# Kernel tuning notes

Hardware: AMD Instinct MI355X
Metric: run time of the kernel (lower is better)

Reference implementation:

```python
import jax, jax.numpy as jnp
import numpy as np

POOL_SCALES = (1, 3, 6, 8)
CHANNELS = 256
BN_EPS = 1e-5


def _pool_matrix(in_size, out_size):
    # Row i averages input slots [floor(i*in/out), ceil((i+1)*in/out)) -- matches AdaptiveAvgPool2d.
    P = np.zeros((out_size, in_size), np.float32)
    for i in range(out_size):
        s = (i * in_size) // out_size
        e = -((-(i + 1) * in_size) // out_size)
        P[i, s:e] = 1.0 / (e - s)
    return jnp.asarray(P)


def _bn(x, g, b, m, v):
    # inference-mode BatchNorm2d on NCHW
    inv = g * jax.lax.rsqrt(v + BN_EPS)
    return x * inv[None, :, None, None] + (b - m * inv)[None, :, None, None]


def _conv1x1(x, w):
    # 1x1 conv == channel matmul: w [Cout, Cin], x [B, Cin, H, W]
    return jnp.einsum('oc,bchw->bohw', w, x)


def _ppm_concat(x):
    # x: [B, C, H, W] -> [B, C, sum(s*s)]
    B, C, H, W = x.shape
    outs = []
    for s in POOL_SCALES:
        Ph = _pool_matrix(H, s)
        Pw = _pool_matrix(W, s)
        pooled = jnp.einsum('ih,jw,bchw->bcij', Ph, Pw, x)
        outs.append(pooled.reshape(B, C, -1))
    return jnp.concatenate(outs, axis=2)


def setup_inputs() -> dict:
    key = jax.random.key(0)
    ks = jax.random.split(key, 24)
    B, Cl, Ch, Cmid, Cout, H, W = 8, 1024, 2048, 256, 2048, 64, 64
    return {
        'low_feats': jax.random.normal(ks[0], (B, Cl, H, W), jnp.float32),
        'high_feats': jax.random.normal(ks[1], (B, Ch, H, W), jnp.float32),
        'q_w': jax.random.normal(ks[2], (Cmid, Ch), jnp.float32) * 0.02,
        'q_g': jax.random.uniform(ks[3], (Cmid,), jnp.float32, 0.5, 1.5),
        'q_b': jax.random.normal(ks[4], (Cmid,), jnp.float32) * 0.1,
        'q_m': jax.random.normal(ks[5], (Cmid,), jnp.float32) * 0.1,
        'q_v': jax.random.uniform(ks[6], (Cmid,), jnp.float32, 0.5, 1.5),
        'k_w': jax.random.normal(ks[7], (Cmid, Cl), jnp.float32) * 0.02,
        'k_g': jax.random.uniform(ks[8], (Cmid,), jnp.float32, 0.5, 1.5),
        'k_b': jax.random.normal(ks[9], (Cmid,), jnp.float32) * 0.1,
        'k_m': jax.random.normal(ks[10], (Cmid,), jnp.float32) * 0.1,
        'k_v': jax.random.uniform(ks[11], (Cmid,), jnp.float32, 0.5, 1.5),
        'v_w': jax.random.normal(ks[12], (Cmid, Cl), jnp.float32) * 0.02,
        'v_b': jax.random.normal(ks[13], (Cmid,), jnp.float32) * 0.02,
        'o_w': jax.random.normal(ks[14], (Cout, Cmid), jnp.float32) * 0.02,
        'o_b': jax.random.normal(ks[15], (Cout,), jnp.float32) * 0.02,
        'bn_w': jax.random.normal(ks[16], (Cout, Cout + Ch), jnp.float32) * 0.02,
        'bn_g': jax.random.uniform(ks[17], (Cout,), jnp.float32, 0.5, 1.5),
        'bn_b': jax.random.normal(ks[18], (Cout,), jnp.float32) * 0.1,
        'bn_m': jax.random.normal(ks[19], (Cout,), jnp.float32) * 0.1,
        'bn_v': jax.random.uniform(ks[20], (Cout,), jnp.float32, 0.5, 1.5),
    }


def reference(low_feats, high_feats, q_w, q_g, q_b, q_m, q_v,
              k_w, k_g, k_b, k_m, k_v, v_w, v_b, o_w, o_b,
              bn_w, bn_g, bn_b, bn_m, bn_v):
    B, _, H, W = high_feats.shape
    # query: ConvModule (1x1 conv, BN, ReLU) on high-level feats; query_scale=1 -> no downsample
    q = jax.nn.relu(_bn(_conv1x1(high_feats, q_w), q_g, q_b, q_m, q_v))
    q = q.reshape(B, CHANNELS, H * W).transpose(0, 2, 1)  # [B, N, C]
    # key: ConvModule then pyramid-pooled; value: plain 1x1 conv then pyramid-pooled
    k = jax.nn.relu(_bn(_conv1x1(low_feats, k_w), k_g, k_b, k_m, k_v))
    k = _ppm_concat(k)  # [B, C, M]
    v = _conv1x1(low_feats, v_w) + v_b[None, :, None, None]
    v = _ppm_concat(v).transpose(0, 2, 1)  # [B, M, C]
    # matmul-normalized attention with pooled K/V (M = 110, tiny)
    sim = jnp.einsum('bnc,bcm->bnm', q, k) * (CHANNELS ** -0.5)
    sim = jax.nn.softmax(sim, axis=-1)
    ctx = jnp.einsum('bnm,bmc->bnc', sim, v)  # [B, N, C]
    ctx = ctx.transpose(0, 2, 1).reshape(B, CHANNELS, H, W)
    # out projection: plain 1x1 conv with bias
    ctx = _conv1x1(ctx, o_w) + o_b[None, :, None, None]  # [B, Cout, H, W]
    # single stage (query_scales=(1,)), stack+sum is identity
    # bottleneck: 1x1 conv (no bias) + BN, no activation
    fused = jnp.concatenate([ctx, high_feats], axis=1)
    out = _bn(_conv1x1(fused, bn_w), bn_g, bn_b, bn_m, bn_v)
    return out
```

## Files before the change

### kernel.cpp

```cpp
#include <hip/hip_runtime.h>
#include <hip/hip_bf16.h>

typedef unsigned int u32;
typedef unsigned short u16;
typedef short s16x8 __attribute__((ext_vector_type(8)));
typedef float f32x4 __attribute__((ext_vector_type(4)));
typedef u16 u16x4 __attribute__((ext_vector_type(4)));

__device__ __forceinline__ u16 f2b(float x) {
  u32 u = __float_as_uint(x);
  return (u16)((u + 0x7fffu + ((u >> 16) & 1u)) >> 16);
}
__device__ __forceinline__ float b2f(u16 x) { return __uint_as_float(((u32)x) << 16); }

__device__ __forceinline__ void gload16(const void* g, void* l) {
  __builtin_amdgcn_global_load_lds((const __attribute__((address_space(1))) u32*)g,
                                   (__attribute__((address_space(3))) u32*)l, 16, 0, 0);
}
__device__ __forceinline__ f32x4 mfma16(s16x8 a, s16x8 b, f32x4 c) {
  return __builtin_amdgcn_mfma_f32_16x16x32_bf16(a, b, c, 0, 0, 0);
}

template <int OUT_BF16>
__global__ __launch_bounds__(512, 2) void gemm256(
    const u16* __restrict__ A, long long sA, int lda,
    const u16* __restrict__ B1, long long sB1, int K1,
    const u16* __restrict__ B2, long long sB2, int K2,
    void* __restrict__ Cv, long long sC, int ldc,
    const float* __restrict__ bias, int bias_mode,
    int relu_limit, float alpha) {
  const int K = K1 + K2, nt = K >> 6;
  int tm, tn, b;
  {
    const int flat = blockIdx.x + gridDim.x * (blockIdx.y + gridDim.y * blockIdx.z);
    if (gridDim.z == 8) {
      const int slot = flat >> 3;
      b = flat & 7;
      tm = slot % gridDim.x;
      tn = slot / gridDim.x;
    } else { tm = blockIdx.x; tn = blockIdx.y; b = blockIdx.z; }
  }
  const u16* Ab = A + (size_t)b * sA + (size_t)tm * 256 * lda;
  const u16* B1b = B1 + (size_t)b * sB1 + (size_t)tn * 256 * K1;
  const u16* B2b = B2 ? (B2 + (size_t)b * sB2 + (size_t)tn * 256 * K2) : (const u16*)0;

  __shared__ __attribute__((aligned(128))) char lds[131072];

  const int tt = threadIdx.x, w = tt >> 6, l = tt & 63;
  const int wr = w >> 2, wc = w & 3;
  const int lr = l & 15, g16 = l >> 4;
  const int sxl = (lr & 7) << 4;

  auto stage_Aq = [&](int kt, int q) {
    const int bufB = (kt & 1) << 16;
    const int kk = kt << 6;
    const int lin = tt << 4;
    const int x = lin ^ (((lin >> 7) & 7) << 4);
    gload16(Ab + (size_t)((q << 6) + (x >> 7)) * lda + kk + ((x & 127) >> 1),
            lds + bufB + (q << 13) + (w << 10));
  };
  auto stage_Bh = [&](int kt, int h) {
    const int bufB = (kt & 1) << 16;
    const int kk = kt << 6;
    const u16* src; int ld, kcol;
    if (kk < K1) { src = B1b; ld = K1; kcol = kk; }
    else         { src = B2b; ld = K2; kcol = kk - K1; }
#pragma unroll
    for (int g = 0; g < 2; ++g) {
      const int lin = (g << 13) | (tt << 4);
      const int x = lin ^ (((lin >> 7) & 7) << 4);
      gload16(src + (size_t)((h << 7) + (x >> 7)) * ld + kcol + ((x & 127) >> 1),
              lds + bufB + 32768 + (h << 14) + (g << 13) + (w << 10));
    }
  };

  auto lda_frag = [&](const char* Al, int h, int kk, s16x8* af) {
#pragma unroll
    for (int i = 0; i < 4; ++i) {
      const int row = wr * 128 + (h * 4 + i) * 16 + lr;
      af[i] = *reinterpret_cast<const s16x8*>(
          Al + (row << 7) + (((kk << 6) | (g16 << 4)) ^ sxl));
    }
  };
  auto ldb_frag = [&](const char* Bl, int kk, s16x8* bf) {
#pragma unroll
    for (int n = 0; n < 4; ++n) {
      const int row = wc * 64 + n * 16 + lr;
      bf[n] = *reinterpret_cast<const s16x8*>(
          Bl + (row << 7) + (((kk << 6) | (g16 << 4)) ^ sxl));
    }
  };

  f32x4 acc[8][4] = {};

  auto mfma_q = [&](int h, const s16x8* af, const s16x8* bf) {
    __builtin_amdgcn_s_setprio(1);
#pragma unroll
    for (int i = 0; i < 4; ++i)
#pragma unroll
      for (int n = 0; n < 4; ++n)
        acc[h * 4 + i][n] = mfma16(af[i], bf[n], acc[h * 4 + i][n]);
    __builtin_amdgcn_s_setprio(0);
  };

  stage_Aq(0, 0); stage_Aq(0, 2); stage_Bh(0, 0); stage_Bh(0, 1);
  stage_Aq(0, 1); stage_Aq(0, 3);
  if (nt > 1) {
    stage_Aq(1, 0); stage_Aq(1, 2); stage_Bh(1, 0); stage_Bh(1, 1);
    asm volatile("s_waitcnt vmcnt(6)" ::: "memory");
  } else {
    asm volatile("s_waitcnt vmcnt(0)" ::: "memory");
  }
  __builtin_amdgcn_s_barrier();

  for (int t = 0; t < nt; ++t) {
    const char* Al = lds + ((t & 1) << 16);
    const char* Bl = Al + 32768;
    s16x8 bf0[4], bf1[4], af[4];

    lda_frag(Al, 0, 0, af);
    ldb_frag(Bl, 0, bf0);
    if (t + 1 < nt) { stage_Aq(t + 1, 1); stage_Aq(t + 1, 3); }
    __builtin_amdgcn_s_barrier();
    asm volatile("s_waitcnt lgkmcnt(0)" ::: "memory");
    mfma_q(0, af, bf0);
    __builtin_amdgcn_s_barrier();

    lda_frag(Al, 0, 1, af);
    ldb_frag(Bl, 1, bf1);
    __builtin_amdgcn_s_barrier();
    asm volatile("s_waitcnt lgkmcnt(0)" ::: "memory");
    mfma_q(0, af, bf1);
    __builtin_amdgcn_s_barrier();

    lda_frag(Al, 1, 0, af);
    if (t + 2 < nt) { stage_Aq(t + 2, 0); stage_Aq(t + 2, 2); stage_Bh(t + 2, 0); }
    __builtin_amdgcn_s_barrier();
    asm volatile("s_waitcnt lgkmcnt(0)" ::: "memory");
    mfma_q(1, af, bf0);
    __builtin_amdgcn_s_barrier();

    lda_frag(Al, 1, 1, af);
    if (t + 2 < nt) stage_Bh(t + 2, 1);
    __builtin_amdgcn_s_barrier();
    asm volatile("s_waitcnt lgkmcnt(0)" ::: "memory");
    mfma_q(1, af, bf1);
    if (t + 1 < nt) {
      if (t + 2 < nt) asm volatile("s_waitcnt vmcnt(6)" ::: "memory");
      else            asm volatile("s_waitcnt vmcnt(0)" ::: "memory");
    }
    __builtin_amdgcn_s_barrier();
  }

  const int li = g16 * 4;
#pragma unroll
  for (int m = 0; m < 8; ++m) {
    const int row = tm * 256 + wr * 128 + m * 16 + li;
#pragma unroll
    for (int j = 0; j < 4; ++j) {
      const int col = tn * 256 + wc * 64 + j * 16 + lr;
      const float bc = (bias_mode == 1) ? bias[col] : 0.f;
#pragma unroll
      for (int i = 0; i < 4; ++i) {
        float v = acc[m][j][i] * alpha;
        v += (bias_mode == 2) ? bias[row + i] : bc;
        if (col < relu_limit) v = fmaxf(v, 0.f);
        const size_t idx = (size_t)b * sC + (size_t)(row + i) * ldc + col;
        if (OUT_BF16) ((u16*)Cv)[idx] = f2b(v);
        else          ((float*)Cv)[idx] = v;
      }
    }
  }
}

template <int OUT_BF16>
__global__ __launch_bounds__(256) void gemm_bt(
    const u16* __restrict__ A, long long sA, int lda,
    const u16* __restrict__ B1, long long sB1, int K1,
    const u16* __restrict__ B2, long long sB2, int K2,
    void* __restrict__ Cv, long long sC, int ldc,
    const float* __restrict__ bias, int bias_mode,
    int relu_limit, float alpha) {
  const int K = K1 + K2;
  const int b = blockIdx.z;
  const int tm = blockIdx.x, tn = blockIdx.y;
  const u16* Ab = A + (size_t)b * sA;
  const u16* B1b = B1 + (size_t)b * sB1;
  const u16* B2b = B2 ? (B2 + (size_t)b * sB2) : (const u16*)0;

  __shared__ u16 As[128 * 32];
  __shared__ u16 Bs[128 * 32];

  const int t = threadIdx.x;
  const int w = t >> 6, l = t & 63;
  const int wr = w >> 1, wc = w & 1;
  const int srow = w * 16 + (l >> 2);
  const int scol = (l & 3) * 8;
  u16* AsW = As + w * 512;
  u16* BsW = Bs + w * 512;

  f32x4 acc[4][4] = {};
  const int lr = l & 15, lk = (l >> 4) * 8;

  for (int kk = 0; kk < K; kk += 32) {
    __syncthreads();
    {
      const u16* g0 = Ab + (size_t)(tm * 128 + srow) * lda + (kk + scol);
      gload16(g0, AsW);
      gload16(g0 + (size_t)64 * lda, AsW + 2048);
    }
    {
      const u16* bb; int ld, kloc;
      if (kk < K1) { bb = B1b; ld = K1; kloc = kk; }
      else         { bb = B2b; ld = K2; kloc = kk - K1; }
      const u16* g0 = bb + (size_t)(tn * 128 + srow) * ld + (kloc + scol);
      gload16(g0, BsW);
      gload16(g0 + (size_t)64 * ld, BsW + 2048);
    }
    __syncthreads();
    s16x8 af[4], bfr[4];
#pragma unroll
    for (int m = 0; m < 4; ++m)
      af[m] = *reinterpret_cast<const s16x8*>(&As[(wr * 64 + m * 16 + lr) * 32 + lk]);
#pragma unroll
    for (int j = 0; j < 4; ++j)
      bfr[j] = *reinterpret_cast<const s16x8*>(&Bs[(wc * 64 + j * 16 + lr) * 32 + lk]);
#pragma unroll
    for (int m = 0; m < 4; ++m)
#pragma unroll
      for (int j = 0; j < 4; ++j)
        acc[m][j] = mfma16(af[m], bfr[j], acc[m][j]);
  }

  const int li = (l >> 4) * 4;
#pragma unroll
  for (int m = 0; m < 4; ++m) {
    const int row = tm * 128 + wr * 64 + m * 16 + li;
#pragma unroll
    for (int j = 0; j < 4; ++j) {
      const int col = tn * 128 + wc * 64 + j * 16 + lr;
      const float bc = (bias_mode == 1) ? bias[col] : 0.f;
#pragma unroll
      for (int i = 0; i < 4; ++i) {
        float v = acc[m][j][i] * alpha;
        v += (bias_mode == 2) ? bias[row + i] : bc;
        if (col < relu_limit) v = fmaxf(v, 0.f);
        const size_t idx = (size_t)b * sC + (size_t)(row + i) * ldc + col;
        if (OUT_BF16) ((u16*)Cv)[idx] = f2b(v);
        else          ((float*)Cv)[idx] = v;
      }
    }
  }
}

__global__ __launch_bounds__(512) void attn_fused(
    const u16* __restrict__ qT,
    const u16* __restrict__ Kp,
    const u16* __restrict__ Vp,
    u16* __restrict__ ctxT) {
  const int qb = blockIdx.x, b = blockIdx.y;
  const int tt = threadIdx.x, w = tt >> 6, l = tt & 63;
  const int lr = l & 15, hi = l >> 4;
  __shared__ __attribute__((aligned(128))) char lds[131072];

  const char* KpG = (const char*)(Kp + (size_t)b * 32768);
  const char* VpG = (const char*)(Vp + (size_t)b * 32768);
#pragma unroll
  for (int g = 0; g < 8; ++g) {
    const int lin = (g * 512 + tt) << 4;
    gload16(KpG + (lin ^ (((lin >> 9) & 7) << 4)), lds + g * 8192 + w * 1024);
  }
#pragma unroll
  for (int g = 0; g < 8; ++g) {
    const int lin = (g * 512 + tt) << 4;
    gload16(VpG + (lin ^ (((lin >> 8) & 7) << 4)), lds + 65536 + g * 8192 + w * 1024);
  }

  const u16* qG = qT + ((size_t)b * 4096 + qb * 128 + w * 16 + lr) * 256 + hi * 8;
  s16x8 qf[8];
#pragma unroll
  for (int kk = 0; kk < 8; ++kk)
    qf[kk] = *reinterpret_cast<const s16x8*>(qG + kk * 32);

  asm volatile("s_waitcnt vmcnt(0)" ::: "memory");
  __syncthreads();

  f32x4 ps[8] = {};
  for (int kk = 0; kk < 8; ++kk) {
#pragma unroll
    for (int j = 0; j < 8; ++j) {
      const int y = (j * 16 + lr) * 512 + kk * 64 + hi * 16;
      const s16x8 kf = *reinterpret_cast<const s16x8*>(lds + (y ^ (((y >> 9) & 7) << 4)));
      ps[j] = mfma16(qf[kk], kf, ps[j]);
    }
  }
  __syncthreads();

#pragma unroll
  for (int i = 0; i < 4; ++i) {
    float m0 = -1e30f;
#pragma unroll
    for (int j = 0; j < 7; ++j) {
      float v = ps[j][i] * 0.0625f;
      if (j == 6 && lr >= 14) v = -1e30f;
      m0 = fmaxf(m0, v);
    }
#pragma unroll
    for (int off = 8; off; off >>= 1) m0 = fmaxf(m0, __shfl_xor(m0, off, 16));
    float s0 = 0.f;
#pragma unroll
    for (int j = 0; j < 7; ++j) {
      const float v = ps[j][i] * 0.0625f;
      const float ev = (j == 6 && lr >= 14) ? 0.f : __expf(v - m0);
      ps[j][i] = ev;
      s0 += ev;
    }
    ps[7][i] = 0.f;
#pragma unroll
    for (int off = 8; off; off >>= 1) s0 += __shfl_xor(s0, off, 16);
    const float inv = 1.f / s0;
#pragma unroll
    for (int j = 0; j < 8; ++j) ps[j][i] *= inv;
  }

  char* PL = lds + w * 4096;
#pragma unroll
  for (int j = 0; j < 8; ++j)
#pragma unroll
    for (int i = 0; i < 4; ++i) {
      const int n = hi * 4 + i, m = j * 16 + lr;
      const int y = n * 256 + m * 2;
      *reinterpret_cast<u16*>(PL + (y ^ ((n & 7) << 4))) = f2b(ps[j][i]);
    }
  __syncthreads();

  f32x4 pc[16] = {};
  const char* VL = lds + 65536;
#pragma unroll
  for (int kk = 0; kk < 4; ++kk) {
    const int ya = lr * 256 + kk * 64 + hi * 16;
    const s16x8 pa = *reinterpret_cast<const s16x8*>(PL + (ya ^ ((lr & 7) << 4)));
#pragma unroll
    for (int jc = 0; jc < 16; ++jc) {
      const int y = (jc * 16 + lr) * 256 + kk * 64 + hi * 16;
      const s16x8 vf = *reinterpret_cast<const s16x8*>(VL + (y ^ (((y >> 8) & 7) << 4)));
      pc[jc] = mfma16(pa, vf, pc[jc]);
    }
  }

  u16* outp = ctxT + ((size_t)b * 4096 + qb * 128 + w * 16) * 256;
#pragma unroll
  for (int jc = 0; jc < 16; ++jc)
#pragma unroll
    for (int i = 0; i < 4; ++i)
      outp[(size_t)(hi * 4 + i) * 256 + jc * 16 + lr] = f2b(pc[jc][i]);
}

__global__ __launch_bounds__(256) void transpose_cvt(
    const float* __restrict__ in, u16* __restrict__ out, int R, int C) {
  const int b = blockIdx.z;
  in += (size_t)b * R * C;
  out += (size_t)b * R * C;
  const int ct = blockIdx.x, rt = blockIdx.y;
  __shared__ float tile[64][65];
  const int t = threadIdx.x;
  {
    const int c4 = (t & 15) * 4, r0 = t >> 4;
    const float* src = in + (size_t)(rt * 64 + r0) * C + ct * 64 + c4;
#pragma unroll
    for (int i = 0; i < 4; ++i) {
      const float4 v = *reinterpret_cast<const float4*>(src + (size_t)(i * 16) * C);
      tile[r0 + i * 16][c4 + 0] = v.x; tile[r0 + i * 16][c4 + 1] = v.y;
      tile[r0 + i * 16][c4 + 2] = v.z; tile[r0 + i * 16][c4 + 3] = v.w;
    }
  }
  __syncthreads();
  {
    const int r4 = (t & 15) * 4, c0 = t >> 4;
    u16* dst = out + (size_t)(ct * 64 + c0) * R + rt * 64 + r4;
#pragma unroll
    for (int i = 0; i < 4; ++i) {
      u16x4 o;
      o.x = f2b(tile[r4 + 0][c0 + i * 16]);
      o.y = f2b(tile[r4 + 1][c0 + i * 16]);
      o.z = f2b(tile[r4 + 2][c0 + i * 16]);
      o.w = f2b(tile[r4 + 3][c0 + i * 16]);
      *reinterpret_cast<u16x4*>(dst + (size_t)(i * 16) * R) = o;
    }
  }
}

__global__ __launch_bounds__(256) void prep_wq(const float* __restrict__ qw,
    const float* __restrict__ qg, const float* __restrict__ qb_,
    const float* __restrict__ qm, const float* __restrict__ qv,
    u16* __restrict__ Wq, float* __restrict__ qbias) {
  const int i = blockIdx.x * 256 + threadIdx.x;
  const int o = i >> 11, c = i & 2047;
  const float inv = qg[o] * rsqrtf(qv[o] + 1e-5f);
  Wq[i] = f2b(qw[i] * inv);
  if (c == 0) qbias[o] = qb_[o] - qm[o] * inv;
}

__global__ __launch_bounds__(256) void prep_wkv(const float* __restrict__ kw,
    const float* __restrict__ kg, const float* __restrict__ kb,
    const float* __restrict__ km, const float* __restrict__ kv,
    const float* __restrict__ vw, const float* __restrict__ vb,
    u16* __restrict__ Wkv, float* __restrict__ kvbias) {
  const int i = blockIdx.x * 256 + threadIdx.x;
  const int r = i >> 10, c = i & 1023;
  if (r < 256) {
    const float inv = kg[r] * rsqrtf(kv[r] + 1e-5f);
    Wkv[i] = f2b(kw[i] * inv);
    if (c == 0) kvbias[r] = kb[r] - km[r] * inv;
  } else {
    Wkv[i] = f2b(vw[(size_t)(r - 256) * 1024 + c]);
    if (c == 0) kvbias[r] = vb[r - 256];
  }
}

__global__ __launch_bounds__(256) void prep_bn(const float* __restrict__ bn_w,
    const float* __restrict__ g, const float* __restrict__ v_,
    u16* __restrict__ bn1s, u16* __restrict__ Wfin) {
  const int i = blockIdx.x * 256 + threadIdx.x;
  const int o = i >> 11, j = i & 2047;
  const float inv = g[o] * rsqrtf(v_[o] + 1e-5f);
  bn1s[i] = f2b(bn_w[(size_t)o * 4096 + j] * inv);
  Wfin[(size_t)o * 2304 + j] = f2b(bn_w[(size_t)o * 4096 + 2048 + j] * inv);
}

__global__ __launch_bounds__(256) void prep_fbias(const float* __restrict__ bn_w,
    const float* __restrict__ o_b, const float* __restrict__ g,
    const float* __restrict__ bb, const float* __restrict__ m_,
    const float* __restrict__ v_, float* __restrict__ fbias) {
  const int o = blockIdx.x, t = threadIdx.x;
  float s = 0.f;
  for (int j = t; j < 2048; j += 256) s += bn_w[(size_t)o * 4096 + j] * o_b[j];
  for (int off = 32; off; off >>= 1) s += __shfl_xor(s, off);
  __shared__ float red[4];
  if ((t & 63) == 0) red[t >> 6] = s;
  __syncthreads();
  if (t == 0) {
    const float tot = red[0] + red[1] + red[2] + red[3];
    const float inv = g[o] * rsqrtf(v_[o] + 1e-5f);
    fbias[o] = inv * tot + bb[o] - m_[o] * inv;
  }
}

__device__ __forceinline__ void jj_to_range(int jj, int& s, int& j, int& c0, int& c1) {
  if (jj < 1)       { s = 1; j = jj; }
  else if (jj < 4)  { s = 3; j = jj - 1; }
  else if (jj < 10) { s = 6; j = jj - 4; }
  else              { s = 8; j = jj - 10; }
  c0 = (j * 64) / s;
  c1 = ((j + 1) * 64 + s - 1) / s;
}

__global__ __launch_bounds__(256) void pool_cols(const u16* __restrict__ kvT,
                                                 float* __restrict__ cp) {
  const int b = blockIdx.y, r = blockIdx.x, t = threadIdx.x;
  const u16* base = kvT + ((size_t)b * 4096 + (size_t)r * 64) * 512;
  const int ch0 = (t & 63) * 8;
  for (int jj = (t >> 6); jj < 18; jj += 4) {
    int s, j, c0, c1;
    jj_to_range(jj, s, j, c0, c1);
    float acc[8] = {0.f, 0.f, 0.f, 0.f, 0.f, 0.f, 0.f, 0.f};
    for (int c = c0; c < c1; ++c) {
      const s16x8 v = *reinterpret_cast<const s16x8*>(base + (size_t)c * 512 + ch0);
#pragma unroll
      for (int i = 0; i < 8; ++i) acc[i] += b2f((u16)v[i]);
    }
    float* o = cp + (((size_t)(b * 64 + r) * 18 + jj) * 512 + ch0);
    *reinterpret_cast<float4*>(o)     = make_float4(acc[0], acc[1], acc[2], acc[3]);
    *reinterpret_cast<float4*>(o + 4) = make_float4(acc[4], acc[5], acc[6], acc[7]);
  }
}

__global__ __launch_bounds__(256) void pool_rows(const float* __restrict__ cp,
    u16* __restrict__ Kp, u16* __restrict__ Vp) {
  const int b = blockIdx.y, m = blockIdx.x, t = threadIdx.x;
  if (m >= 110) {
    Kp[((size_t)b * 128 + m) * 256 + t] = 0;
    Vp[((size_t)b * 256 + t) * 128 + m] = 0;
    return;
  }
  int s, idx, jjbase;
  if (m < 1)       { s = 1; idx = m;      jjbase = 0; }
  else if (m < 10) { s = 3; idx = m - 1;  jjbase = 1; }
  else if (m < 46) { s = 6; idx = m - 10; jjbase = 4; }
  else             { s = 8; idx = m - 46; jjbase = 10; }
  const int i = idx / s, j = idx % s;
  const int jj = jjbase + j;
  const int r0 = (i * 64) / s, r1 = ((i + 1) * 64 + s - 1) / s;
  const int c0 = (j * 64) / s, c1 = ((j + 1) * 64 + s - 1) / s;
  float a0 = 0.f, a1 = 0.f;
  for (int r = r0; r < r1; ++r) {
    const float* px = cp + ((size_t)(b * 64 + r) * 18 + jj) * 512;
    a0 += px[t];
    a1 += px[t + 256];
  }
  const float inv = 1.f / (float)((r1 - r0) * (c1 - c0));
  Kp[((size_t)b * 128 + m) * 256 + t] = f2b(a0 * inv);
  Vp[((size_t)b * 256 + t) * 128 + m] = f2b(a1 * inv);
}

extern "C" void kernel_launch(void* const* d_in, const int* in_sizes, int n_in,
                              void* d_out, int out_size, void* d_ws, size_t ws_size,
                              hipStream_t stream) {
  (void)in_sizes; (void)n_in; (void)out_size; (void)ws_size;
  const float* low  = (const float*)d_in[0];
  const float* high = (const float*)d_in[1];
  const float* q_w = (const float*)d_in[2];
  const float* q_g = (const float*)d_in[3];
  const float* q_b = (const float*)d_in[4];
  const float* q_m = (const float*)d_in[5];
  const float* q_v = (const float*)d_in[6];
  const float* k_w = (const float*)d_in[7];
  const float* k_g = (const float*)d_in[8];
  const float* k_b = (const float*)d_in[9];
  const float* k_m = (const float*)d_in[10];
  const float* k_v = (const float*)d_in[11];
  const float* v_w = (const float*)d_in[12];
  const float* v_b = (const float*)d_in[13];
  const float* o_w = (const float*)d_in[14];
  const float* o_b = (const float*)d_in[15];
  const float* bn_w = (const float*)d_in[16];
  const float* bn_g = (const float*)d_in[17];
  const float* bn_b = (const float*)d_in[18];
  const float* bn_m = (const float*)d_in[19];
  const float* bn_v = (const float*)d_in[20];
  float* out = (float*)d_out;

  char* ws = (char*)d_ws;
  size_t off = 0;
  auto alloc = [&](size_t bytes) -> char* {
    char* p = ws + off;
    off += (bytes + 255) & ~(size_t)255;
    return p;
  };
  u16* XhT  = (u16*)alloc(134217728ull);
  u16* qT   = (u16*)alloc(16777216ull);
  u16* XlT  = (u16*)alloc(67108864ull);
  u16* kvT  = (u16*)alloc(33554432ull);
  u16* ctxT = (u16*)alloc(16777216ull);
  u16* Kpool = (u16*)alloc(524288ull);
  u16* VpT   = (u16*)alloc(524288ull);
  u16* Wq   = (u16*)alloc(1048576ull);
  u16* Wkv  = (u16*)alloc(1048576ull);
  u16* Wfin = (u16*)alloc(9437184ull);
  float* qbias  = (float*)alloc(1024);
  float* kvbias = (float*)alloc(2048);
  float* fbias  = (float*)alloc(8192);
  u16* bn1s = qT;
  u16* owT  = ctxT;
  float* cp  = (float*)((char*)XlT + 25165824ull);

  prep_bn<<<16384, 256, 0, stream>>>(bn_w, bn_g, bn_v, bn1s, Wfin);
  prep_fbias<<<2048, 256, 0, stream>>>(bn_w, o_b, bn_g, bn_b, bn_m, bn_v, fbias);
  prep_wq<<<2048, 256, 0, stream>>>(q_w, q_g, q_b, q_m, q_v, Wq, qbias);
  prep_wkv<<<2048, 256, 0, stream>>>(k_w, k_g, k_b, k_m, k_v, v_w, v_b, Wkv, kvbias);
  transpose_cvt<<<dim3(4, 32, 1), 256, 0, stream>>>(o_w, owT, 2048, 256);
  gemm_bt<1><<<dim3(16, 2, 1), 256, 0, stream>>>(
      bn1s, 0, 2048, owT, 0, 2048, (const u16*)0, 0, 0,
      (void*)(Wfin + 2048), 0, 2304, (const float*)0, 0, 0, 1.0f);

  transpose_cvt<<<dim3(64, 32, 8), 256, 0, stream>>>(high, XhT, 2048, 4096);
  transpose_cvt<<<dim3(64, 16, 8), 256, 0, stream>>>(low, XlT, 1024, 4096);

  gemm_bt<1><<<dim3(32, 2, 8), 256, 0, stream>>>(
      XhT, 4096ll * 2048, 2048, Wq, 0, 2048, (const u16*)0, 0, 0,
      qT, 4096ll * 256, 256, qbias, 1, 256, 1.0f);
  gemm256<1><<<dim3(16, 2, 8), 512, 0, stream>>>(
      XlT, 4096ll * 1024, 1024, Wkv, 0, 1024, (const u16*)0, 0, 0,
      kvT, 4096ll * 512, 512, kvbias, 1, 256, 1.0f);
  pool_cols<<<dim3(64, 8), 256, 0, stream>>>(kvT, cp);
  pool_rows<<<dim3(128, 8), 256, 0, stream>>>(cp, Kpool, VpT);
  attn_fused<<<dim3(32, 8), 512, 0, stream>>>(qT, Kpool, VpT, ctxT);
  gemm256<0><<<dim3(8, 16, 8), 512, 0, stream>>>(
      Wfin, 0, 2304, XhT, 4096ll * 2048, 2048, ctxT, 4096ll * 256, 256,
      out, 2048ll * 4096, 4096, fbias, 2, 0, 1.0f);
}
```

Baseline: 736.8 us.

## Restructure 256x256 GEMM to four waves with larger per-wave tiles

```diff
diff --git a/kernel.cpp b/kernel.cpp
--- a/kernel.cpp
+++ b/kernel.cpp
@@ -22,7 +22,7 @@
 }
 
 template <int OUT_BF16>
-__global__ __launch_bounds__(512, 2) void gemm256(
+__global__ __launch_bounds__(256, 1) void gemm256w4(
     const u16* __restrict__ A, long long sA, int lda,
     const u16* __restrict__ B1, long long sB1, int K1,
     const u16* __restrict__ B2, long long sB2, int K2,
@@ -47,17 +47,20 @@
   __shared__ __attribute__((aligned(128))) char lds[131072];
 
   const int tt = threadIdx.x, w = tt >> 6, l = tt & 63;
-  const int wr = w >> 2, wc = w & 3;
+  const int wr = w >> 1, wc = w & 1;
   const int lr = l & 15, g16 = l >> 4;
   const int sxl = (lr & 7) << 4;
 
   auto stage_Aq = [&](int kt, int q) {
     const int bufB = (kt & 1) << 16;
     const int kk = kt << 6;
-    const int lin = tt << 4;
-    const int x = lin ^ (((lin >> 7) & 7) << 4);
-    gload16(Ab + (size_t)((q << 6) + (x >> 7)) * lda + kk + ((x & 127) >> 1),
-            lds + bufB + (q << 13) + (w << 10));
+#pragma unroll
+    for (int g = 0; g < 2; ++g) {
+      const int lin = ((g << 8) + tt) << 4;
+      const int x = lin ^ (((lin >> 7) & 7) << 4);
+      gload16(Ab + (size_t)((q << 6) + (x >> 7)) * lda + kk + ((x & 127) >> 1),
+              lds + bufB + (q << 13) + (g << 12) + (w << 10));
+    }
   };
   auto stage_Bh = [&](int kt, int h) {
     const int bufB = (kt & 1) << 16;
@@ -66,48 +69,48 @@
     if (kk < K1) { src = B1b; ld = K1; kcol = kk; }
     else         { src = B2b; ld = K2; kcol = kk - K1; }
 #pragma unroll
-    for (int g = 0; g < 2; ++g) {
-      const int lin = (g << 13) | (tt << 4);
+    for (int g = 0; g < 4; ++g) {
+      const int lin = ((g << 8) + tt) << 4;
       const int x = lin ^ (((lin >> 7) & 7) << 4);
       gload16(src + (size_t)((h << 7) + (x >> 7)) * ld + kcol + ((x & 127) >> 1),
-              lds + bufB + 32768 + (h << 14) + (g << 13) + (w << 10));
+              lds + bufB + 32768 + (h << 14) + (g << 12) + (w << 10));
     }
   };
 
-  auto lda_frag = [&](const char* Al, int h, int kk, s16x8* af) {
+  auto lda4 = [&](const char* Al, int h, int kk1, s16x8* af) {
 #pragma unroll
     for (int i = 0; i < 4; ++i) {
       const int row = wr * 128 + (h * 4 + i) * 16 + lr;
       af[i] = *reinterpret_cast<const s16x8*>(
-          Al + (row << 7) + (((kk << 6) | (g16 << 4)) ^ sxl));
+          Al + (row << 7) + (((kk1 << 6) | (g16 << 4)) ^ sxl));
     }
   };
-  auto ldb_frag = [&](const char* Bl, int kk, s16x8* bf) {
-#pragma unroll
-    for (int n = 0; n < 4; ++n) {
-      const int row = wc * 64 + n * 16 + lr;
+  auto ldb8 = [&](const char* Bl, int kk1, s16x8* bf) {
+#pragma unroll
+    for (int n = 0; n < 8; ++n) {
+      const int row = wc * 128 + n * 16 + lr;
       bf[n] = *reinterpret_cast<const s16x8*>(
-          Bl + (row << 7) + (((kk << 6) | (g16 << 4)) ^ sxl));
+          Bl + (row << 7) + (((kk1 << 6) | (g16 << 4)) ^ sxl));
     }
   };
 
-  f32x4 acc[8][4] = {};
-
-  auto mfma_q = [&](int h, const s16x8* af, const s16x8* bf) {
+  f32x4 acc[8][8] = {};
+
+  auto mfma_hp = [&](int h, const s16x8* af, const s16x8* bf) {
     __builtin_amdgcn_s_setprio(1);
 #pragma unroll
     for (int i = 0; i < 4; ++i)
 #pragma unroll
-      for (int n = 0; n < 4; ++n)
+      for (int n = 0; n < 8; ++n)
         acc[h * 4 + i][n] = mfma16(af[i], bf[n], acc[h * 4 + i][n]);
     __builtin_amdgcn_s_setprio(0);
   };
 
-  stage_Aq(0, 0); stage_Aq(0, 2); stage_Bh(0, 0); stage_Bh(0, 1);
-  stage_Aq(0, 1); stage_Aq(0, 3);
+  stage_Aq(0, 0); stage_Aq(0, 1); stage_Aq(0, 2); stage_Aq(0, 3);
+  stage_Bh(0, 0); stage_Bh(0, 1);
   if (nt > 1) {
-    stage_Aq(1, 0); stage_Aq(1, 2); stage_Bh(1, 0); stage_Bh(1, 1);
-    asm volatile("s_waitcnt vmcnt(6)" ::: "memory");
+    stage_Aq(1, 0); stage_Aq(1, 2);
+    asm volatile("s_waitcnt vmcnt(4)" ::: "memory");
   } else {
     asm volatile("s_waitcnt vmcnt(0)" ::: "memory");
   }
@@ -116,37 +119,38 @@
   for (int t = 0; t < nt; ++t) {
     const char* Al = lds + ((t & 1) << 16);
     const char* Bl = Al + 32768;
-    s16x8 bf0[4], bf1[4], af[4];
-
-    lda_frag(Al, 0, 0, af);
-    ldb_frag(Bl, 0, bf0);
+    s16x8 af[4], bf0[8], bf1[8];
+
+    lda4(Al, 0, 0, af);
+    ldb8(Bl, 0, bf0);
+    if (t + 1 < nt) stage_Bh(t + 1, 0);
+    __builtin_amdgcn_s_barrier();
+    asm volatile("s_waitcnt lgkmcnt(0)" ::: "memory");
+    mfma_hp(0, af, bf0);
+    __builtin_amdgcn_s_barrier();
+
+    lda4(Al, 1, 0, af);
+    if (t + 1 < nt) stage_Bh(t + 1, 1);
+    __builtin_amdgcn_s_barrier();
+    asm volatile("s_waitcnt lgkmcnt(0)" ::: "memory");
+    mfma_hp(1, af, bf0);
+    __builtin_amdgcn_s_barrier();
+
+    lda4(Al, 0, 1, af);
+    ldb8(Bl, 1, bf1);
     if (t + 1 < nt) { stage_Aq(t + 1, 1); stage_Aq(t + 1, 3); }
     __builtin_amdgcn_s_barrier();
     asm volatile("s_waitcnt lgkmcnt(0)" ::: "memory");
-    mfma_q(0, af, bf0);
-    __builtin_amdgcn_s_barrier();
-
-    lda_frag(Al, 0, 1, af);
-    ldb_frag(Bl, 1, bf1);
+    mfma_hp(0, af, bf1);
+    __builtin_amdgcn_s_barrier();
+
+    lda4(Al, 1, 1, af);
+    if (t + 2 < nt) { stage_Aq(t + 2, 0); stage_Aq(t + 2, 2); }
     __builtin_amdgcn_s_barrier();
     asm volatile("s_waitcnt lgkmcnt(0)" ::: "memory");
-    mfma_q(0, af, bf1);
-    __builtin_amdgcn_s_barrier();
-
-    lda_frag(Al, 1, 0, af);
-    if (t + 2 < nt) { stage_Aq(t + 2, 0); stage_Aq(t + 2, 2); stage_Bh(t + 2, 0); }
-    __builtin_amdgcn_s_barrier();
-    asm volatile("s_waitcnt lgkmcnt(0)" ::: "memory");
-    mfma_q(1, af, bf0);
-    __builtin_amdgcn_s_barrier();
-
-    lda_frag(Al, 1, 1, af);
-    if (t + 2 < nt) stage_Bh(t + 2, 1);
-    __builtin_amdgcn_s_barrier();
-    asm volatile("s_waitcnt lgkmcnt(0)" ::: "memory");
-    mfma_q(1, af, bf1);
+    mfma_hp(1, af, bf1);
     if (t + 1 < nt) {
-      if (t + 2 < nt) asm volatile("s_waitcnt vmcnt(6)" ::: "memory");
+      if (t + 2 < nt) asm volatile("s_waitcnt vmcnt(4)" ::: "memory");
       else            asm volatile("s_waitcnt vmcnt(0)" ::: "memory");
     }
     __builtin_amdgcn_s_barrier();
@@ -157,8 +161,8 @@
   for (int m = 0; m < 8; ++m) {
     const int row = tm * 256 + wr * 128 + m * 16 + li;
 #pragma unroll
-    for (int j = 0; j < 4; ++j) {
-      const int col = tn * 256 + wc * 64 + j * 16 + lr;
+    for (int j = 0; j < 8; ++j) {
+      const int col = tn * 256 + wc * 128 + j * 16 + lr;
       const float bc = (bias_mode == 1) ? bias[col] : 0.f;
 #pragma unroll
       for (int i = 0; i < 4; ++i) {
@@ -569,13 +573,13 @@
   gemm_bt<1><<<dim3(32, 2, 8), 256, 0, stream>>>(
       XhT, 4096ll * 2048, 2048, Wq, 0, 2048, (const u16*)0, 0, 0,
       qT, 4096ll * 256, 256, qbias, 1, 256, 1.0f);
-  gemm256<1><<<dim3(16, 2, 8), 512, 0, stream>>>(
+  gemm256w4<1><<<dim3(16, 2, 8), 256, 0, stream>>>(
       XlT, 4096ll * 1024, 1024, Wkv, 0, 1024, (const u16*)0, 0, 0,
       kvT, 4096ll * 512, 512, kvbias, 1, 256, 1.0f);
   pool_cols<<<dim3(64, 8), 256, 0, stream>>>(kvT, cp);
   pool_rows<<<dim3(128, 8), 256, 0, stream>>>(cp, Kpool, VpT);
   attn_fused<<<dim3(32, 8), 512, 0, stream>>>(qT, Kpool, VpT, ctxT);
-  gemm256<0><<<dim3(8, 16, 8), 512, 0, stream>>>(
+  gemm256w4<0><<<dim3(8, 16, 8), 256, 0, stream>>>(
       Wfin, 0, 2304, XhT, 4096ll * 2048, 2048, ctxT, 4096ll * 256, 256,
       out, 2048ll * 4096, 4096, fbias, 2, 0, 1.0f);
 }
```

Result: slower. 843.9 us (+14.5%).
